# Optimization experiments

Measured on AMD Instinct MI355X. Metric: run time of the kernel, lower is better.

Reference implementation:

```python
import jax, jax.numpy as jnp
import numpy as np

NS = 0.4      # neighborhood_size
GS = 8        # grid_size
RNN = 128     # rnn_size
EMB = 64      # embedding_size
NMIX = 20     # nmixtures
N = 1024      # num pedestrians


def setup_inputs() -> dict:
    key = jax.random.key(0)
    ks = jax.random.split(key, 14)
    s = 0.05
    return {
        "xoff": jax.random.normal(ks[0], (N, 2)) * s,
        "xabs": jax.random.uniform(ks[1], (N, 2)),
        "h0": jax.random.normal(ks[2], (1, N, RNN)) * 0.1,
        "c0": jax.random.normal(ks[3], (1, N, RNN)) * 0.1,
        "W_emb": jax.random.normal(ks[4], (EMB, 2)) * s,
        "b_emb": jax.random.normal(ks[5], (EMB,)) * s,
        "W_soc": jax.random.normal(ks[6], (EMB, GS * GS * RNN)) * s,
        "b_soc": jax.random.normal(ks[7], (EMB,)) * s,
        "W_ih": jax.random.normal(ks[8], (4 * RNN, 2 * EMB)) * s,
        "W_hh": jax.random.normal(ks[9], (4 * RNN, RNN)) * s,
        "b_ih": jax.random.normal(ks[10], (4 * RNN,)) * s,
        "b_hh": jax.random.normal(ks[11], (4 * RNN,)) * s,
        "W_out": jax.random.normal(ks[12], (6 * NMIX, RNN)) * s,
        "b_out": jax.random.normal(ks[13], (6 * NMIX,)) * s,
    }


def grid_mask(xabs, dtype):
    # Vectorized getGridMask: [N, N, GS*GS] one-hot neighbor binning.
    x, y = xabs[:, 0], xabs[:, 1]
    dx = x[None, :] - (x[:, None] - NS / 2)  # other_x - width_low, [N, N]
    dy = y[None, :] - (y[:, None] - NS / 2)
    cx = jnp.floor(dx / NS * GS).astype(jnp.int32)
    cy = jnp.floor(dy / NS * GS).astype(jnp.int32)
    n = x.shape[0]
    valid = ((dx >= 0) & (dx < NS) & (dy >= 0) & (dy < NS)
             & (cx >= 0) & (cx < GS) & (cy >= 0) & (cy < GS)
             & ~jnp.eye(n, dtype=bool))
    cell = jnp.clip(cx + cy * GS, 0, GS * GS - 1)
    return jax.nn.one_hot(cell, GS * GS, dtype=dtype) * valid[..., None].astype(dtype)


def reference(xoff, xabs, h0, c0, W_emb, b_emb, W_soc, b_soc,
              W_ih, W_hh, b_ih, b_hh, W_out, b_out):
    n = xabs.shape[0]
    # predict_distance=True -> embed offsets
    emb = jax.nn.relu(xoff @ W_emb.T + b_emb)                 # [N, 64]
    grid = grid_mask(xabs, emb.dtype)                          # [N, N, 64]
    h = h0[0]                                                  # [N, 128]
    # getSocialTensor: scatter neighbor hidden states into grid bins
    social = jnp.einsum('nmg,mh->ngh', grid, h).reshape(n, GS * GS * RNN)
    pool = jax.nn.relu(social @ W_soc.T + b_soc)               # [N, 64]
    xin = jnp.concatenate([emb, pool], axis=-1)                # [N, 128]
    # single-step LSTM, torch gate order i, f, g, o
    gates = xin @ W_ih.T + h @ W_hh.T + b_ih + b_hh            # [N, 512]
    i, f, g, o = jnp.split(gates, 4, axis=-1)
    c = jax.nn.sigmoid(f) * c0[0] + jax.nn.sigmoid(i) * jnp.tanh(g)
    hn = jax.nn.sigmoid(o) * jnp.tanh(c)
    out = hn @ W_out.T + b_out                                 # [N, 120]
    mu1, mu2, ls1, ls2, rho, pi_logits = jnp.split(out, 6, axis=1)
    return (mu1, mu2, ls1, ls2, rho, pi_logits)
```

## Files before the change

kernel.cpp:

```cpp
#include <hip/hip_runtime.h>
#include <hip/hip_bf16.h>

#define NN_ 1024

#define U_WGF  0
#define U_WOUT 131072
#define U_SHI  147456
#define U_SLO  671744
#define U_ACTH 1196032
#define U_ACTL 1458176
#define U_P    1720320
#define F_GL   2957312

typedef __attribute__((ext_vector_type(8))) short short8;
typedef __attribute__((ext_vector_type(4))) float floatx4;

__device__ __forceinline__ float b2f_(unsigned short u) {
    return __uint_as_float(((unsigned)u) << 16);
}
__device__ __forceinline__ unsigned short f2bu(float f) {
    __hip_bfloat16 b = __float2bfloat16(f);
    return *(unsigned short*)&b;
}
__device__ __forceinline__ float ldin(const void* p, int i, int isbf) {
    return isbf ? b2f_(((const unsigned short*)p)[i]) : ((const float*)p)[i];
}
__device__ __forceinline__ int detect_bf16(const void* Wih, int tid) {
    unsigned wv = ((const unsigned*)Wih)[tid];
    unsigned e8 = (wv >> 7) & 0xFFu;
    return (__syncthreads_count((e8 >= 96u && e8 <= 134u) ? 1 : 0) > 128) ? 1 : 0;
}

__global__ __launch_bounds__(256) void prep_kernel(
        const void* __restrict__ xoff, const void* __restrict__ h0,
        const void* __restrict__ Wsoc, const void* __restrict__ Wemb,
        const void* __restrict__ bemb, const void* __restrict__ Wih,
        const void* __restrict__ Whh,  const void* __restrict__ Wout,
        float* __restrict__ ws) {
    const int tid = threadIdx.x;
    const int isbf = detect_bf16(Wih, tid);
    unsigned short* u = (unsigned short*)ws;
    int t = blockIdx.x * 256 + tid;
    if (t < 131072) {
        int r = t & 7, jl = (t >> 3) & 15, q = (t >> 7) & 3;
        int kb = (t >> 9) & 7, jt = t >> 12;
        int j = jt * 16 + jl, k = kb * 32 + q * 8 + r;
        float v = (k < 128) ? ldin(Wih, j * 128 + k, isbf)
                            : ldin(Whh, j * 128 + (k - 128), isbf);
        u[U_WGF + t] = f2bu(v);
    } else if (t < 147456) {
        int t2 = t - 131072; int r = t2 >> 7, j = t2 & 127;
        u[U_WOUT + t2] = f2bu((j < 120) ? ldin(Wout, j * 128 + r, isbf) : 0.0f);
    } else if (t < 671744) {
        int t2 = t - 147456;
        int r = t2 & 7, e = (t2 >> 3) & 63, q = (t2 >> 9) & 3;
        int j = (t2 >> 11) & 3, g = t2 >> 13;
        float x = ldin(Wsoc, e * 8192 + g * 128 + j * 32 + q * 8 + r, isbf);
        unsigned short hi = f2bu(x);
        u[U_SHI + t2] = hi;
        u[U_SLO + t2] = f2bu(x - b2f_(hi));
    } else if (t < 802816) {
        int t2 = t - 671744; int n = t2 >> 7, k = t2 & 127;
        float x = ldin(h0, t2, isbf);
        unsigned short hi = f2bu(x);
        u[U_ACTH + n * 256 + 128 + k] = hi;
        u[U_ACTL + n * 256 + 128 + k] = f2bu(x - b2f_(hi));
    } else {
        int t2 = t - 802816; int n = t2 >> 6, e = t2 & 63;
        float v = fmaf(ldin(xoff, 2 * n, isbf),     ldin(Wemb, 2 * e, isbf),
                  fmaf(ldin(xoff, 2 * n + 1, isbf), ldin(Wemb, 2 * e + 1, isbf),
                       ldin(bemb, e, isbf)));
        v = fmaxf(v, 0.0f);
        unsigned short hi = f2bu(v);
        u[U_ACTH + n * 256 + e] = hi;
        u[U_ACTL + n * 256 + e] = f2bu(v - b2f_(hi));
    }
}

__global__ __launch_bounds__(256) void pgemm_kernel(float* __restrict__ ws) {
    const unsigned short* u = (const unsigned short*)ws;
    const short* Ah  = (const short*)(u + U_ACTH);
    const short* Al  = (const short*)(u + U_ACTL);
    const short* Shi = (const short*)(u + U_SHI);
    const short* Slo = (const short*)(u + U_SLO);
    unsigned short* P16 = (unsigned short*)ws + U_P;
    const int tid = threadIdx.x, lane = tid & 63, wv = tid >> 6;
    const int B_ = blockIdx.y * 64 + blockIdx.x;
    const int mtile = B_ & 63, rest = B_ >> 6;
    const int cg = rest >> 1, thalf = rest & 1;
    const int m = lane & 15, q = lane >> 4;
    const int g = cg * 4 + wv;
    const int abase = (mtile * 16 + m) * 256 + 128 + q * 8;
    short8 ah[4], al[4];
#pragma unroll
    for (int j = 0; j < 4; j++) {
        ah[j] = *(const short8*)(Ah + abase + 32 * j);
        al[j] = *(const short8*)(Al + abase + 32 * j);
    }
    const int rowl = mtile * 16 + q * 4;
#pragma unroll
    for (int tt = 0; tt < 2; tt++) {
        const int t = thalf * 2 + tt;
        const int e = t * 16 + m;
        short8 bh[4], bl[4];
#pragma unroll
        for (int j = 0; j < 4; j++) {
            const int fb = ((g * 4 + j) * 4 + q) * 512 + e * 8;
            bh[j] = *(const short8*)(Shi + fb);
            bl[j] = *(const short8*)(Slo + fb);
        }
        floatx4 c = {0.0f, 0.0f, 0.0f, 0.0f};
#pragma unroll
        for (int j = 0; j < 4; j++) c = __builtin_amdgcn_mfma_f32_16x16x32_bf16(ah[j], bh[j], c, 0, 0, 0);
#pragma unroll
        for (int j = 0; j < 4; j++) c = __builtin_amdgcn_mfma_f32_16x16x32_bf16(ah[j], bl[j], c, 0, 0, 0);
#pragma unroll
        for (int j = 0; j < 4; j++) c = __builtin_amdgcn_mfma_f32_16x16x32_bf16(al[j], bh[j], c, 0, 0, 0);
        const int n0 = cg * 256 + wv * 64 + t * 16;
#pragma unroll
        for (int r = 0; r < 4; r++)
            P16[(rowl + r) * 4096 + n0 + m] = f2bu(c[r]);
    }
}

__global__ __launch_bounds__(256) void pool_kernel(const void* __restrict__ xabs,
                                                   const void* __restrict__ b_soc,
                                                   const void* __restrict__ Wih_det,
                                                   float* __restrict__ ws) {
    __shared__ float xabs_s[2048];
    __shared__ int   off[NN_];
    __shared__ int   cnt_s;
    __shared__ float4 red4[16][16];
    const int tid = threadIdx.x;
    const int isbf = detect_bf16(Wih_det, tid);
    const int n = blockIdx.x;
    unsigned short* u = (unsigned short*)ws;

    for (int i = tid; i < 2048; i += 256) xabs_s[i] = ldin(xabs, i, isbf);
    if (tid == 0) cnt_s = 0;
    __syncthreads();
    {
        float xs = xabs_s[2 * n]     - 0.2f;
        float ys = xabs_s[2 * n + 1] - 0.2f;
        for (int i = tid; i < NN_; i += 256) {
            float dx = xabs_s[2 * i]     - xs;
            float dy = xabs_s[2 * i + 1] - ys;
            int cx = (int)floorf(dx / 0.4f * 8.0f);
            int cy = (int)floorf(dy / 0.4f * 8.0f);
            bool valid = (dx >= 0.0f) && (dx < 0.4f) && (dy >= 0.0f) && (dy < 0.4f)
                      && (cx >= 0) && (cx < 8) && (cy >= 0) && (cy < 8) && (i != n);
            if (valid) {
                int idx = atomicAdd(&cnt_s, 1);
                off[idx] = i * 4096 + ((cy * 8 + cx) << 6);
            }
        }
    }
    __syncthreads();
    {
        const unsigned short* P16 = (const unsigned short*)ws + U_P;
        const int strm = tid >> 4, e4 = tid & 15;
        const int cc = cnt_s;
        float ax = 0.0f, ay = 0.0f, az = 0.0f, aw = 0.0f;
        for (int j = strm; j < cc; j += 16) {
            int o = off[j];
            ushort4 uu = *(const ushort4*)(P16 + o + 4 * e4);
            ax += b2f_(uu.x); ay += b2f_(uu.y); az += b2f_(uu.z); aw += b2f_(uu.w);
        }
        red4[strm][e4] = make_float4(ax, ay, az, aw);
    }
    __syncthreads();
    if (tid < 16) {
        float s[4] = {0.0f, 0.0f, 0.0f, 0.0f};
#pragma unroll
        for (int s16 = 0; s16 < 16; s16++) {
            float4 r = red4[s16][tid];
            s[0] += r.x; s[1] += r.y; s[2] += r.z; s[3] += r.w;
        }
        int e = 4 * tid;
#pragma unroll
        for (int i = 0; i < 4; i++) {
            float v = fmaxf(s[i] + ldin(b_soc, e + i, isbf), 0.0f);
            unsigned short hi = f2bu(v);
            u[U_ACTH + n * 256 + 64 + e + i] = hi;
            u[U_ACTL + n * 256 + 64 + e + i] = f2bu(v - b2f_(hi));
        }
    }
}

__global__ __launch_bounds__(256) void gates_kernel(const void* __restrict__ b_ih,
                                                    const void* __restrict__ b_hh,
                                                    const void* __restrict__ Wih_det,
                                                    float* __restrict__ ws) {
    const int tid = threadIdx.x;
    const int isbf = detect_bf16(Wih_det, tid);
    const unsigned short* u = (const unsigned short*)ws;
    const short* Ah = (const short*)(u + U_ACTH);
    const short* Al = (const short*)(u + U_ACTL);
    const short* Wg = (const short*)(u + U_WGF);
    float* gl = ws + F_GL;
    const int lane = tid & 63, wv = tid >> 6, m = lane & 15, q = lane >> 4;
    const int m0 = blockIdx.x * 16;
    const int jt = blockIdx.y * 4 + wv;
    floatx4 acc = {0.0f, 0.0f, 0.0f, 0.0f};
#pragma unroll
    for (int kb = 0; kb < 8; kb++) {
        const int ab = (m0 + m) * 256 + kb * 32 + q * 8;
        short8 ah = *(const short8*)(Ah + ab);
        short8 al = *(const short8*)(Al + ab);
        short8 b  = *(const short8*)(Wg + (jt * 8 + kb) * 512 + q * 128 + m * 8);
        acc = __builtin_amdgcn_mfma_f32_16x16x32_bf16(ah, b, acc, 0, 0, 0);
        acc = __builtin_amdgcn_mfma_f32_16x16x32_bf16(al, b, acc, 0, 0, 0);
    }
    const int j = jt * 16 + m;
    const float bias = ldin(b_ih, j, isbf) + ldin(b_hh, j, isbf);
#pragma unroll
    for (int r = 0; r < 4; r++)
        gl[(m0 + q * 4 + r) * 512 + j] = acc[r] + bias;
}

__global__ __launch_bounds__(256) void pwout_kernel(const void* __restrict__ c0,
                                                    const void* __restrict__ b_out,
                                                    const void* __restrict__ Wih_det,
                                                    const float* __restrict__ ws,
                                                    float* __restrict__ out) {
    __shared__ __align__(16) float hnl[2][128];
    const int tid = threadIdx.x;
    const int isbf = detect_bf16(Wih_det, tid);
    const int n0 = blockIdx.x * 2;
    const unsigned short* u = (const unsigned short*)ws;
    const float* gl = ws + F_GL;
    const int half = tid >> 7, t2 = tid & 127;
    const int n = n0 + half;
    {
        int r = t2;
        float iv = gl[n * 512 + r],       fv = gl[n * 512 + r + 128];
        float gv = gl[n * 512 + r + 256], ov = gl[n * 512 + r + 384];
        float si = 1.0f / (1.0f + expf(-iv));
        float sf = 1.0f / (1.0f + expf(-fv));
        float so = 1.0f / (1.0f + expf(-ov));
        float cc = sf * ldin(c0, n * 128 + r, isbf) + si * tanhf(gv);
        hnl[half][r] = so * tanhf(cc);
    }
    __syncthreads();
    {
        int j = t2;
        if (j < 120) {
            float acc = ldin(b_out, j, isbf);
            for (int r = 0; r < 128; r += 4) {
                float4 hq = *(const float4*)&hnl[half][r];
                acc = fmaf(hq.x, b2f_(u[U_WOUT + (r + 0) * 128 + j]), acc);
                acc = fmaf(hq.y, b2f_(u[U_WOUT + (r + 1) * 128 + j]), acc);
                acc = fmaf(hq.z, b2f_(u[U_WOUT + (r + 2) * 128 + j]), acc);
                acc = fmaf(hq.w, b2f_(u[U_WOUT + (r + 3) * 128 + j]), acc);
            }
            int ch = j / 20, wc = j - ch * 20;
            out[ch * 20480 + n * 20 + wc] = acc;
        }
    }
}

extern "C" void kernel_launch(void* const* d_in, const int* in_sizes, int n_in,
                              void* d_out, int out_size, void* d_ws, size_t ws_size,
                              hipStream_t stream) {
    const void* xoff  = d_in[0];
    const void* xabs  = d_in[1];
    const void* h0    = d_in[2];
    const void* c0    = d_in[3];
    const void* W_emb = d_in[4];
    const void* b_emb = d_in[5];
    const void* W_soc = d_in[6];
    const void* b_soc = d_in[7];
    const void* W_ih  = d_in[8];
    const void* W_hh  = d_in[9];
    const void* b_ih  = d_in[10];
    const void* b_hh  = d_in[11];
    const void* W_out = d_in[12];
    const void* b_out = d_in[13];
    float* ws = (float*)d_ws;
    float* out = (float*)d_out;

    prep_kernel<<<3392, 256, 0, stream>>>(xoff, h0, W_soc, W_emb, b_emb,
                                          W_ih, W_hh, W_out, ws);
    pgemm_kernel<<<dim3(64, 32), 256, 0, stream>>>(ws);
    pool_kernel<<<1024, 256, 0, stream>>>(xabs, b_soc, W_ih, ws);
    gates_kernel<<<dim3(64, 8), 256, 0, stream>>>(b_ih, b_hh, W_ih, ws);
    pwout_kernel<<<512, 256, 0, stream>>>(c0, b_out, W_ih, ws, out);
}
```

Measured before the change: 125.2 us.

## Fuse LSTM gate GEMM, pointwise cell update, and output projection into one kernel

Merges the gates MFMA kernel and the pointwise/output kernel into one kernel, one block per 16 rows. Gate pre-activations stay in padded shared memory instead of a global scratch buffer, which removes a kernel launch and a global write/read round trip. Each block now computes all 512 gate columns by looping over 8 tiles per wave with the A fragments kept in registers. The grid shrinks from 512 blocks to 64, which lowers parallelism on a GPU with many CUs.

```diff
diff --git a/kernel.cpp b/kernel.cpp
--- a/kernel.cpp
+++ b/kernel.cpp
@@ -10,7 +10,6 @@
 #define U_ACTH 1196032
 #define U_ACTL 1458176
 #define U_P    1720320
-#define F_GL   2957312
 
 typedef __attribute__((ext_vector_type(8))) short short8;
 typedef __attribute__((ext_vector_type(4))) float floatx4;
@@ -187,74 +186,69 @@
     }
 }
 
-__global__ __launch_bounds__(256) void gates_kernel(const void* __restrict__ b_ih,
-                                                    const void* __restrict__ b_hh,
-                                                    const void* __restrict__ Wih_det,
-                                                    float* __restrict__ ws) {
+__global__ __launch_bounds__(256) void gates_out_kernel(
+        const void* __restrict__ c0,   const void* __restrict__ b_ih,
+        const void* __restrict__ b_hh, const void* __restrict__ b_out,
+        const void* __restrict__ Wih_det,
+        const float* __restrict__ ws, float* __restrict__ out) {
+    __shared__ float gl[16 * 516];
+    __shared__ __align__(16) float hnl[16][128];
     const int tid = threadIdx.x;
     const int isbf = detect_bf16(Wih_det, tid);
     const unsigned short* u = (const unsigned short*)ws;
     const short* Ah = (const short*)(u + U_ACTH);
     const short* Al = (const short*)(u + U_ACTL);
     const short* Wg = (const short*)(u + U_WGF);
-    float* gl = ws + F_GL;
     const int lane = tid & 63, wv = tid >> 6, m = lane & 15, q = lane >> 4;
     const int m0 = blockIdx.x * 16;
-    const int jt = blockIdx.y * 4 + wv;
-    floatx4 acc = {0.0f, 0.0f, 0.0f, 0.0f};
+    short8 ah[8], al[8];
 #pragma unroll
     for (int kb = 0; kb < 8; kb++) {
         const int ab = (m0 + m) * 256 + kb * 32 + q * 8;
-        short8 ah = *(const short8*)(Ah + ab);
-        short8 al = *(const short8*)(Al + ab);
-        short8 b  = *(const short8*)(Wg + (jt * 8 + kb) * 512 + q * 128 + m * 8);
-        acc = __builtin_amdgcn_mfma_f32_16x16x32_bf16(ah, b, acc, 0, 0, 0);
-        acc = __builtin_amdgcn_mfma_f32_16x16x32_bf16(al, b, acc, 0, 0, 0);
-    }
-    const int j = jt * 16 + m;
-    const float bias = ldin(b_ih, j, isbf) + ldin(b_hh, j, isbf);
-#pragma unroll
-    for (int r = 0; r < 4; r++)
-        gl[(m0 + q * 4 + r) * 512 + j] = acc[r] + bias;
-}
-
-__global__ __launch_bounds__(256) void pwout_kernel(const void* __restrict__ c0,
-                                                    const void* __restrict__ b_out,
-                                                    const void* __restrict__ Wih_det,
-                                                    const float* __restrict__ ws,
-                                                    float* __restrict__ out) {
-    __shared__ __align__(16) float hnl[2][128];
-    const int tid = threadIdx.x;
-    const int isbf = detect_bf16(Wih_det, tid);
-    const int n0 = blockIdx.x * 2;
-    const unsigned short* u = (const unsigned short*)ws;
-    const float* gl = ws + F_GL;
-    const int half = tid >> 7, t2 = tid & 127;
-    const int n = n0 + half;
-    {
-        int r = t2;
-        float iv = gl[n * 512 + r],       fv = gl[n * 512 + r + 128];
-        float gv = gl[n * 512 + r + 256], ov = gl[n * 512 + r + 384];
+        ah[kb] = *(const short8*)(Ah + ab);
+        al[kb] = *(const short8*)(Al + ab);
+    }
+#pragma unroll
+    for (int tt = 0; tt < 8; tt++) {
+        const int jt = tt * 4 + wv;
+        floatx4 acc = {0.0f, 0.0f, 0.0f, 0.0f};
+#pragma unroll
+        for (int kb = 0; kb < 8; kb++) {
+            short8 b = *(const short8*)(Wg + (jt * 8 + kb) * 512 + q * 128 + m * 8);
+            acc = __builtin_amdgcn_mfma_f32_16x16x32_bf16(ah[kb], b, acc, 0, 0, 0);
+            acc = __builtin_amdgcn_mfma_f32_16x16x32_bf16(al[kb], b, acc, 0, 0, 0);
+        }
+        const int j = jt * 16 + m;
+        const float bias = ldin(b_ih, j, isbf) + ldin(b_hh, j, isbf);
+#pragma unroll
+        for (int r = 0; r < 4; r++)
+            gl[(q * 4 + r) * 516 + j] = acc[r] + bias;
+    }
+    __syncthreads();
+    for (int i = tid; i < 2048; i += 256) {
+        int a = i >> 7, r = i & 127;
+        float iv = gl[a * 516 + r],       fv = gl[a * 516 + r + 128];
+        float gv = gl[a * 516 + r + 256], ov = gl[a * 516 + r + 384];
         float si = 1.0f / (1.0f + expf(-iv));
         float sf = 1.0f / (1.0f + expf(-fv));
         float so = 1.0f / (1.0f + expf(-ov));
-        float cc = sf * ldin(c0, n * 128 + r, isbf) + si * tanhf(gv);
-        hnl[half][r] = so * tanhf(cc);
-    }
-    __syncthreads();
-    {
-        int j = t2;
+        float cc = sf * ldin(c0, (m0 + a) * 128 + r, isbf) + si * tanhf(gv);
+        hnl[a][r] = so * tanhf(cc);
+    }
+    __syncthreads();
+    for (int i = tid; i < 2048; i += 256) {
+        int a = i >> 7, j = i & 127;
         if (j < 120) {
             float acc = ldin(b_out, j, isbf);
             for (int r = 0; r < 128; r += 4) {
-                float4 hq = *(const float4*)&hnl[half][r];
+                float4 hq = *(const float4*)&hnl[a][r];
                 acc = fmaf(hq.x, b2f_(u[U_WOUT + (r + 0) * 128 + j]), acc);
                 acc = fmaf(hq.y, b2f_(u[U_WOUT + (r + 1) * 128 + j]), acc);
                 acc = fmaf(hq.z, b2f_(u[U_WOUT + (r + 2) * 128 + j]), acc);
                 acc = fmaf(hq.w, b2f_(u[U_WOUT + (r + 3) * 128 + j]), acc);
             }
             int ch = j / 20, wc = j - ch * 20;
-            out[ch * 20480 + n * 20 + wc] = acc;
+            out[ch * 20480 + (m0 + a) * 20 + wc] = acc;
         }
     }
 }
@@ -283,6 +277,5 @@
                                           W_ih, W_hh, W_out, ws);
     pgemm_kernel<<<dim3(64, 32), 256, 0, stream>>>(ws);
     pool_kernel<<<1024, 256, 0, stream>>>(xabs, b_soc, W_ih, ws);
-    gates_kernel<<<dim3(64, 8), 256, 0, stream>>>(b_ih, b_hh, W_ih, ws);
-    pwout_kernel<<<512, 256, 0, stream>>>(c0, b_out, W_ih, ws, out);
-}
+    gates_out_kernel<<<64, 256, 0, stream>>>(c0, b_ih, b_hh, b_out, W_ih, ws, out);
+}
```

Result: slower. 231.0 us (+84.5%).
